# Kernel tuning notes

Hardware: AMD Instinct MI355X
Metric: run time of the kernel (lower is better)

Reference implementation:

```python
import jax, jax.numpy as jnp
import numpy as np

G = 128   # long_term_attn_g
H = 8     # num_attn_heads


def setup_inputs() -> dict:
    key = jax.random.key(0)
    ks = jax.random.split(key, 8)
    b, d, t, dk = 8, 1024, 8192, 512  # dk = model_dim // 2
    return {
        "qk": jax.random.normal(ks[0], (b, d, t), jnp.float32),
        "masks": jnp.ones((b, 1, t), jnp.float32),
        "wq": jax.random.normal(ks[1], (dk, d), jnp.float32) * 0.02,
        "bq": jnp.zeros((dk,), jnp.float32),
        "wk": jax.random.normal(ks[2], (dk, d), jnp.float32) * 0.02,
        "bk": jnp.zeros((dk,), jnp.float32),
        "wv": jax.random.normal(ks[3], (dk, d), jnp.float32) * 0.02,
        "bv": jnp.zeros((dk,), jnp.float32),
        "wo": jax.random.normal(ks[4], (d, dk), jnp.float32) * 0.02,
        "bo": jnp.zeros((d,), jnp.float32),
    }


def _to_patches(x, g):
    # convert_to_patches + rearrange 'b d np p -> (b p) d np'
    b, d, t = x.shape
    pad = (-t) % g
    x = jnp.pad(x, ((0, 0), (0, 0), (0, pad)))
    npat = x.shape[-1] // g
    return x.reshape(b, d, npat, g).transpose(0, 3, 1, 2).reshape(b * g, d, npat)


def reference(qk, masks, wq, bq, wk, bk, wv, bv, wo, bo):
    b, d, t = qk.shape
    xp = _to_patches(qk, G)     # [(b g), d, npat]  -- q, k, v source
    mp = _to_patches(masks, G)  # [(b g), 1, npat]  -- key-side attention mask

    # pointwise Conv1d projections == per-timestep matmuls
    q = jnp.einsum('od,bdt->bot', wq, xp) + bq[:, None]
    k = jnp.einsum('od,bdt->bot', wk, xp) + bk[:, None]
    v = jnp.einsum('od,bdt->bot', wv, xp) + bv[:, None]

    dk = wq.shape[0]
    dh = dk // H
    bg, _, npat = q.shape
    qh = q.reshape(bg, H, dh, npat)
    kh = k.reshape(bg, H, dh, npat)
    vh = v.reshape(bg, H, dh, npat)

    scores = jnp.einsum('bhdi,bhdj->bhij', qh, kh) / jnp.sqrt(jnp.float32(dh))
    scores = jnp.where(mp[:, :, None, :] > 0, scores, jnp.float32(-1e9))
    attn = jax.nn.softmax(scores, axis=-1)
    out = jnp.einsum('bhij,bhdj->bhdi', attn, vh).reshape(bg, dk, npat)

    # out_proj = GELU -> Conv1d(dk -> model_dim, k=1)
    out = jax.nn.gelu(out, approximate=False)
    out = jnp.einsum('od,bdt->bot', wo, out) + bo[:, None]

    # undo reshape: '(b g) d np -> b d (np g)', trim padding
    out = out.reshape(b, G, d, npat).transpose(0, 2, 3, 1).reshape(b, d, npat * G)[:, :, :t]
    return out * masks
```

## Files before the change

kernel.cpp:

```cpp
#include <hip/hip_runtime.h>
#include <hip/hip_bf16.h>
#include <cmath>

typedef __attribute__((ext_vector_type(4))) float f32x4;
typedef __attribute__((ext_vector_type(8))) short s16x8;

typedef __attribute__((address_space(1))) const void glb_void_t;
typedef __attribute__((address_space(3))) void lds_void_t;

#define MFMA(a, b, c) __builtin_amdgcn_mfma_f32_16x16x32_bf16(a, b, c, 0, 0, 0)
#define GLOAD_LDS(g, l) __builtin_amdgcn_global_load_lds((glb_void_t*)(g), (lds_void_t*)(l), 16, 0, 0)

__device__ __forceinline__ unsigned short bf(float x) {
  union { float f; unsigned u; } c; c.f = x;
  unsigned r = (c.u + 0x7fffu + ((c.u >> 16) & 1u)) >> 16;
  return (unsigned short)r;
}

__global__ void k_prep(const float* __restrict__ wq, const float* __restrict__ wk,
                       const float* __restrict__ wv, const float* __restrict__ bq,
                       const float* __restrict__ bk, const float* __restrict__ bv,
                       const float* __restrict__ wo,
                       __hip_bfloat16* __restrict__ wqkv, __hip_bfloat16* __restrict__ wob,
                       float* __restrict__ bqkv) {
  const int NW = 1536 * 1024, NO = 1024 * 512;
  for (int i = blockIdx.x * blockDim.x + threadIdx.x; i < NW + NO + 1536;
       i += gridDim.x * blockDim.x) {
    if (i < NW) {
      int r = i >> 10;
      float v = (r < 512) ? wq[i] : ((r < 1024) ? wk[i - 512 * 1024] : wv[i - 1024 * 1024]);
      ((unsigned short*)wqkv)[i] = bf(v);
    } else if (i < NW + NO) {
      int j = i - NW;
      ((unsigned short*)wob)[j] = bf(wo[j]);
    } else {
      int j = i - NW - NO;
      bqkv[j] = (j < 512) ? bq[j] : ((j < 1024) ? bk[j - 512] : bv[j - 1024]);
    }
  }
}

__global__ __launch_bounds__(256) void k_transpose(const float* __restrict__ qk,
                                                   __hip_bfloat16* __restrict__ qkT) {
  __shared__ float tile[64][65];
  const int b = blockIdx.z, t0 = blockIdx.x * 64, d0 = blockIdx.y * 64;
  const int tid = threadIdx.x;
  const int tq = tid & 15, dr = tid >> 4;
  const float* src = qk + ((size_t)b * 1024 + d0) * 8192 + t0;
#pragma unroll
  for (int i = 0; i < 4; i++) {
    int d = dr + i * 16;
    float4 v = *(const float4*)(src + (size_t)d * 8192 + tq * 4);
    tile[d][tq * 4 + 0] = v.x; tile[d][tq * 4 + 1] = v.y;
    tile[d][tq * 4 + 2] = v.z; tile[d][tq * 4 + 3] = v.w;
  }
  __syncthreads();
  const int d4 = (tid & 15) * 4, tr = tid >> 4;
  unsigned short* dst = (unsigned short*)qkT + ((size_t)b * 8192 + t0) * 1024 + d0;
#pragma unroll
  for (int i = 0; i < 4; i++) {
    int t = tr + i * 16;
    ushort4 o4;
    o4.x = bf(tile[d4 + 0][t]); o4.y = bf(tile[d4 + 1][t]);
    o4.z = bf(tile[d4 + 2][t]); o4.w = bf(tile[d4 + 3][t]);
    *(ushort4*)(dst + (size_t)t * 1024 + d4) = o4;
  }
}

__device__ __forceinline__ void stage_half(char* lds_base, const char* gbase,
                                           int ktile, int w, int l) {
#pragma unroll
  for (int r = 0; r < 2; ++r) {
    int row = r * 64 + w * 8 + (l >> 3);
    int cb = ((l & 7) * 16) ^ ((row & 7) << 4);
    GLOAD_LDS(gbase + (size_t)row * 2048 + (size_t)ktile * 128 + cb,
              lds_base + (r * 64 + w * 8) * 128);
  }
}

__global__ __launch_bounds__(512, 2) void k_qkv(const __hip_bfloat16* __restrict__ qkT,
                                                const __hip_bfloat16* __restrict__ wqkv,
                                                const float* __restrict__ bqkv,
                                                __hip_bfloat16* __restrict__ qkv) {
  __shared__ char smem[131072];
  const int NT = 16;
  const int b = blockIdx.z, t0 = blockIdx.x * 256, o0 = blockIdx.y * 256;
  const int tid = threadIdx.x, l = tid & 63, w = tid >> 6;
  const int c = l & 15, g = l >> 4;
  const int wm = w >> 2, wn = w & 3;
  const int cbase = (g * 16) ^ ((c & 7) << 4);
  const int brow = (wn & 1) * 64;

  const char* qpanel = (const char*)qkT + ((size_t)b * 8192 + t0) * 2048;
  const char* wpanel = (const char*)wqkv + (size_t)o0 * 2048;

#define STAGE_B2(tt) { stage_half(smem + 65536 + ((tt)&1) * 32768, wpanel, (tt), w, l); \
                       stage_half(smem + 65536 + ((tt)&1) * 32768 + 16384, wpanel + 262144, (tt), w, l); }
#define STAGE_A2(tt) { stage_half(smem + ((tt)&1) * 32768, qpanel, (tt), w, l); \
                       stage_half(smem + ((tt)&1) * 32768 + 16384, qpanel + 262144, (tt), w, l); }

  f32x4 acc[8][4];
#pragma unroll
  for (int i = 0; i < 8; i++)
#pragma unroll
    for (int j = 0; j < 4; j++) acc[i][j] = (f32x4){0.f, 0.f, 0.f, 0.f};

  STAGE_B2(0); STAGE_A2(0); STAGE_B2(1); STAGE_A2(1);
  asm volatile("s_waitcnt vmcnt(8)" ::: "memory");
  __builtin_amdgcn_s_barrier();
  __builtin_amdgcn_sched_barrier(0);

  s16x8 avLo[4][2], avHi[4][2], bvLo[2][2], bvHi[2][2];
  {
    const char* Ah = smem + wm * 16384;
    const char* Bh = smem + 65536 + (wn >> 1) * 16384;
#pragma unroll
    for (int mi = 0; mi < 4; ++mi)
#pragma unroll
      for (int kk = 0; kk < 2; ++kk)
        avLo[mi][kk] = *(const s16x8*)(Ah + (mi * 16 + c) * 128 + (cbase ^ (kk << 6)));
#pragma unroll
    for (int ni = 0; ni < 2; ++ni)
#pragma unroll
      for (int kk = 0; kk < 2; ++kk)
        bvLo[ni][kk] = *(const s16x8*)(Bh + (brow + ni * 16 + c) * 128 + (cbase ^ (kk << 6)));
  }

#pragma unroll 2
  for (int t = 0; t < NT; ++t) {
    const int buf = t & 1;
    const char* Ah = smem + buf * 32768 + wm * 16384;
    const char* Bh = smem + 65536 + buf * 32768 + (wn >> 1) * 16384;
    const char* Ah2 = smem + (buf ^ 1) * 32768 + wm * 16384;
    const char* Bh2 = smem + 65536 + (buf ^ 1) * 32768 + (wn >> 1) * 16384;

#pragma unroll
    for (int ni = 0; ni < 2; ++ni)
#pragma unroll
      for (int kk = 0; kk < 2; ++kk)
        bvHi[ni][kk] = *(const s16x8*)(Bh + (brow + (2 + ni) * 16 + c) * 128 + (cbase ^ (kk << 6)));
#pragma unroll
    for (int mi = 0; mi < 2; ++mi)
#pragma unroll
      for (int kk = 0; kk < 2; ++kk)
        avHi[mi][kk] = *(const s16x8*)(Ah + (64 + mi * 16 + c) * 128 + (cbase ^ (kk << 6)));
    __builtin_amdgcn_s_barrier();
    asm volatile("s_waitcnt lgkmcnt(8)" ::: "memory");
    __builtin_amdgcn_sched_barrier(0);
    __builtin_amdgcn_s_setprio(1);
#pragma unroll
    for (int mi = 0; mi < 4; ++mi)
#pragma unroll
      for (int ni = 0; ni < 2; ++ni)
#pragma unroll
        for (int kk = 0; kk < 2; ++kk)
          acc[mi][ni] = MFMA(avLo[mi][kk], bvLo[ni][kk], acc[mi][ni]);
    __builtin_amdgcn_s_setprio(0);
    __builtin_amdgcn_s_barrier();

#pragma unroll
    for (int mi = 2; mi < 4; ++mi)
#pragma unroll
      for (int kk = 0; kk < 2; ++kk)
        avHi[mi][kk] = *(const s16x8*)(Ah + (64 + mi * 16 + c) * 128 + (cbase ^ (kk << 6)));
    __builtin_amdgcn_s_barrier();
    asm volatile("s_waitcnt lgkmcnt(8)" ::: "memory");
    __builtin_amdgcn_sched_barrier(0);
    __builtin_amdgcn_s_setprio(1);
#pragma unroll
    for (int mi = 0; mi < 4; ++mi)
#pragma unroll
      for (int ni = 0; ni < 2; ++ni)
#pragma unroll
        for (int kk = 0; kk < 2; ++kk)
          acc[mi][ni + 2] = MFMA(avLo[mi][kk], bvHi[ni][kk], acc[mi][ni + 2]);
    __builtin_amdgcn_s_setprio(0);
    __builtin_amdgcn_s_barrier();

    if (t + 2 < NT) STAGE_B2(t + 2);
    __builtin_amdgcn_s_barrier();
    asm volatile("s_waitcnt lgkmcnt(0)" ::: "memory");
    __builtin_amdgcn_sched_barrier(0);
    __builtin_amdgcn_s_setprio(1);
#pragma unroll
    for (int mi = 0; mi < 4; ++mi)
#pragma unroll
      for (int ni = 0; ni < 2; ++ni)
#pragma unroll
        for (int kk = 0; kk < 2; ++kk)
          acc[mi + 4][ni] = MFMA(avHi[mi][kk], bvLo[ni][kk], acc[mi + 4][ni]);
    __builtin_amdgcn_s_setprio(0);
    __builtin_amdgcn_s_barrier();

    if (t + 2 < NT) STAGE_A2(t + 2);
    if (t + 2 < NT) {
      asm volatile("s_waitcnt vmcnt(8)" ::: "memory");
    } else {
      asm volatile("s_waitcnt vmcnt(0)" ::: "memory");
    }
    __builtin_amdgcn_s_barrier();
    __builtin_amdgcn_sched_barrier(0);
    if (t + 1 < NT) {
#pragma unroll
      for (int mi = 0; mi < 4; ++mi)
#pragma unroll
        for (int kk = 0; kk < 2; ++kk)
          avLo[mi][kk] = *(const s16x8*)(Ah2 + (mi * 16 + c) * 128 + (cbase ^ (kk << 6)));
#pragma unroll
      for (int ni = 0; ni < 2; ++ni)
#pragma unroll
        for (int kk = 0; kk < 2; ++kk)
          bvLo[ni][kk] = *(const s16x8*)(Bh2 + (brow + ni * 16 + c) * 128 + (cbase ^ (kk << 6)));
    }
    __builtin_amdgcn_s_setprio(1);
#pragma unroll
    for (int mi = 0; mi < 4; ++mi)
#pragma unroll
      for (int ni = 0; ni < 2; ++ni)
#pragma unroll
        for (int kk = 0; kk < 2; ++kk)
          acc[mi + 4][ni + 2] = MFMA(avHi[mi][kk], bvHi[ni][kk], acc[mi + 4][ni + 2]);
    __builtin_amdgcn_s_setprio(0);
    __builtin_amdgcn_s_barrier();
  }
#undef STAGE_A2
#undef STAGE_B2

  unsigned short* outb = (unsigned short*)qkv + ((size_t)b * 8192 + t0) * 1536 + o0;
  float bias[4];
#pragma unroll
  for (int ni = 0; ni < 4; ni++) bias[ni] = bqkv[o0 + wn * 64 + ni * 16 + c];
#pragma unroll
  for (int mi = 0; mi < 8; mi++)
#pragma unroll
    for (int r = 0; r < 4; r++) {
      int t = wm * 128 + mi * 16 + g * 4 + r;
#pragma unroll
      for (int ni = 0; ni < 4; ni++) {
        int o = wn * 64 + ni * 16 + c;
        outb[(size_t)t * 1536 + o] = bf(acc[mi][ni][r] + bias[ni]);
      }
    }
}

__global__ __launch_bounds__(64) void k_attn(const __hip_bfloat16* __restrict__ qkv,
                                             const float* __restrict__ masks,
                                             __hip_bfloat16* __restrict__ a_out) {
  const int l = threadIdx.x, c = l & 15, g = l >> 4;
  const int h = blockIdx.x & 7, bg = blockIdx.x >> 3;
  const int gg = bg & 127, b = bg >> 7;
  const size_t rowstep = (size_t)128 * 1536;
  const __hip_bfloat16* base = qkv + ((size_t)b * 8192 + gg) * 1536 + h * 64;
  const __hip_bfloat16* Qb = base;
  const __hip_bfloat16* Kb = base + 512;
  const __hip_bfloat16* Vb = base + 1024;

  s16x8 kf[4][2], qf[4][2];
#pragma unroll
  for (int f = 0; f < 4; f++)
#pragma unroll
    for (int kk = 0; kk < 2; kk++) {
      size_t roff = (size_t)(f * 16 + c) * rowstep + kk * 32 + g * 8;
      kf[f][kk] = *(const s16x8*)(Kb + roff);
      qf[f][kk] = *(const s16x8*)(Qb + roff);
    }
  f32x4 st[4][4];
#pragma unroll
  for (int i = 0; i < 4; i++)
#pragma unroll
    for (int j = 0; j < 4; j++) st[i][j] = (f32x4){0.f, 0.f, 0.f, 0.f};
#pragma unroll
  for (int mj = 0; mj < 4; mj++)
#pragma unroll
    for (int ni = 0; ni < 4; ni++)
#pragma unroll
      for (int kk = 0; kk < 2; kk++)
        st[mj][ni] = MFMA(kf[mj][kk], qf[ni][kk], st[mj][ni]);

  float mk[4][4];
#pragma unroll
  for (int mj = 0; mj < 4; mj++)
#pragma unroll
    for (int r = 0; r < 4; r++)
      mk[mj][r] = masks[(size_t)b * 8192 + (size_t)(mj * 16 + g * 4 + r) * 128 + gg];

  float inv[4];
#pragma unroll
  for (int ni = 0; ni < 4; ni++) {
    float m = -1e30f;
#pragma unroll
    for (int mj = 0; mj < 4; mj++)
#pragma unroll
      for (int r = 0; r < 4; r++) {
        float s = st[mj][ni][r] * 0.125f;
        s = (mk[mj][r] > 0.f) ? s : -1e9f;
        st[mj][ni][r] = s;
        m = fmaxf(m, s);
      }
    m = fmaxf(m, __shfl_xor(m, 16));
    m = fmaxf(m, __shfl_xor(m, 32));
    float sm = 0.f;
#pragma unroll
    for (int mj = 0; mj < 4; mj++)
#pragma unroll
      for (int r = 0; r < 4; r++) {
        float p = expf(st[mj][ni][r] - m);
        st[mj][ni][r] = p;
        sm += p;
      }
    sm += __shfl_xor(sm, 16);
    sm += __shfl_xor(sm, 32);
    inv[ni] = 1.f / sm;
  }
#pragma unroll
  for (int mj = 0; mj < 4; mj++)
#pragma unroll
    for (int ni = 0; ni < 4; ni++)
#pragma unroll
      for (int r = 0; r < 4; r++) st[mj][ni][r] *= inv[ni];

  unsigned qd[4][4][2];
#pragma unroll
  for (int ni = 0; ni < 4; ni++)
#pragma unroll
    for (int mj = 0; mj < 4; mj++)
#pragma unroll
      for (int wv = 0; wv < 2; wv++)
        qd[ni][mj][wv] = (unsigned)bf(st[mj][ni][2 * wv]) |
                         ((unsigned)bf(st[mj][ni][2 * wv + 1]) << 16);

  f32x4 oacc[4][4];
#pragma unroll
  for (int i = 0; i < 4; i++)
#pragma unroll
    for (int j = 0; j < 4; j++) oacc[i][j] = (f32x4){0.f, 0.f, 0.f, 0.f};

  const int srcA = c + 32 * (g & 1);
  const int srcB = srcA + 16;
  const bool hi = (g >= 2);
#pragma unroll
  for (int kk = 0; kk < 2; kk++) {
    s16x8 af[4];
#pragma unroll
    for (int ni = 0; ni < 4; ni++) {
      unsigned a0 = __shfl(qd[ni][2 * kk][0], srcA);
      unsigned b0 = __shfl(qd[ni][2 * kk + 1][0], srcA);
      unsigned a1 = __shfl(qd[ni][2 * kk][1], srcA);
      unsigned b1 = __shfl(qd[ni][2 * kk + 1][1], srcA);
      unsigned a2 = __shfl(qd[ni][2 * kk][0], srcB);
      unsigned b2 = __shfl(qd[ni][2 * kk + 1][0], srcB);
      unsigned a3 = __shfl(qd[ni][2 * kk][1], srcB);
      unsigned b3 = __shfl(qd[ni][2 * kk + 1][1], srcB);
      union { unsigned u[4]; s16x8 v; } uu;
      uu.u[0] = hi ? b0 : a0;
      uu.u[1] = hi ? b1 : a1;
      uu.u[2] = hi ? b2 : a2;
      uu.u[3] = hi ? b3 : a3;
      af[ni] = uu.v;
    }
    s16x8 bvv[4];
#pragma unroll
    for (int fd = 0; fd < 4; fd++) {
      s16x8 t;
#pragma unroll
      for (int e = 0; e < 8; e++)
        t[e] = *(const short*)(Vb + (size_t)(kk * 32 + g * 8 + e) * rowstep + fd * 16 + c);
      bvv[fd] = t;
    }
#pragma unroll
    for (int fi = 0; fi < 4; fi++)
#pragma unroll
      for (int fd = 0; fd < 4; fd++)
        oacc[fi][fd] = MFMA(af[fi], bvv[fd], oacc[fi][fd]);
  }

  unsigned short* ob = (unsigned short*)a_out + ((size_t)b * 8192 + gg) * 512 + h * 64;
#pragma unroll
  for (int fi = 0; fi < 4; fi++)
#pragma unroll
    for (int fd = 0; fd < 4; fd++)
#pragma unroll
      for (int r = 0; r < 4; r++) {
        float x = oacc[fi][fd][r];
        float ge = 0.5f * x * (1.f + erff(x * 0.70710678118f));
        int i = fi * 16 + g * 4 + r;
        ob[(size_t)i * (128 * 512) + fd * 16 + c] = bf(ge);
      }
}

__global__ __launch_bounds__(512) void k_out(const __hip_bfloat16* __restrict__ wob,
                                             const __hip_bfloat16* __restrict__ a,
                                             const float* __restrict__ bo,
                                             const float* __restrict__ masks,
                                             float* __restrict__ y) {
  __shared__ char smem[256 * 128 + 128 * 128];
  char* As = smem;
  char* Bs = smem + 32768;
  const int b = blockIdx.z, t0 = blockIdx.x * 128, o0 = blockIdx.y * 256;
  const int tid = threadIdx.x, l = tid & 63, w = tid >> 6;
  const int c = l & 15, g = l >> 4;
  const int wm = w >> 1, wn = w & 1;
  const int lrow = l >> 3, lcol = (l & 7) * 16;

  f32x4 acc[4][4];
#pragma unroll
  for (int i = 0; i < 4; i++)
#pragma unroll
    for (int j = 0; j < 4; j++) acc[i][j] = (f32x4){0.f, 0.f, 0.f, 0.f};

  const char* wbase = (const char*)(wob + (size_t)o0 * 512);
  const char* abase = (const char*)(a + ((size_t)b * 8192 + t0) * 512);

  for (int ks = 0; ks < 8; ks++) {
    __syncthreads();
#pragma unroll
    for (int ii = 0; ii < 4; ii++) {
      int row = w * 32 + ii * 8 + lrow;
      int cb = lcol ^ ((row & 7) << 4);
      const char* gp = wbase + (size_t)row * 1024 + ks * 128 + cb;
      GLOAD_LDS(gp, As + (w * 32 + ii * 8) * 128);
    }
#pragma unroll
    for (int ii = 0; ii < 2; ii++) {
      int row = w * 16 + ii * 8 + lrow;
      int cb = lcol ^ ((row & 7) << 4);
      const char* gp = abase + (size_t)row * 1024 + ks * 128 + cb;
      GLOAD_LDS(gp, Bs + (w * 16 + ii * 8) * 128);
    }
    __syncthreads();
#pragma unroll
    for (int kk = 0; kk < 2; kk++) {
      s16x8 av[4], bv[4];
#pragma unroll
      for (int mi = 0; mi < 4; mi++) {
        int row = wm * 64 + mi * 16 + c;
        int cb = (kk * 64 + g * 16) ^ ((row & 7) << 4);
        av[mi] = *(const s16x8*)(As + row * 128 + cb);
      }
#pragma unroll
      for (int ni = 0; ni < 4; ni++) {
        int row = wn * 64 + ni * 16 + c;
        int cb = (kk * 64 + g * 16) ^ ((row & 7) << 4);
        bv[ni] = *(const s16x8*)(Bs + row * 128 + cb);
      }
#pragma unroll
      for (int mi = 0; mi < 4; mi++)
#pragma unroll
        for (int ni = 0; ni < 4; ni++)
          acc[mi][ni] = MFMA(av[mi], bv[ni], acc[mi][ni]);
    }
  }
  int tcol[4];
  float mk[4];
#pragma unroll
  for (int ni = 0; ni < 4; ni++) {
    tcol[ni] = t0 + wn * 64 + ni * 16 + c;
    mk[ni] = masks[(size_t)b * 8192 + tcol[ni]];
  }
#pragma unroll
  for (int mi = 0; mi < 4; mi++)
#pragma unroll
    for (int r = 0; r < 4; r++) {
      int od = o0 + wm * 64 + mi * 16 + g * 4 + r;
      float bias = bo[od];
      float* yrow = y + ((size_t)b * 1024 + od) * 8192;
#pragma unroll
      for (int ni = 0; ni < 4; ni++)
        yrow[tcol[ni]] = (acc[mi][ni][r] + bias) * mk[ni];
    }
}

extern "C" void kernel_launch(void* const* d_in, const int* in_sizes, int n_in,
                              void* d_out, int out_size, void* d_ws, size_t ws_size,
                              hipStream_t stream) {
  const float* qk = (const float*)d_in[0];
  const float* masks = (const float*)d_in[1];
  const float* wq = (const float*)d_in[2];
  const float* bq = (const float*)d_in[3];
  const float* wk = (const float*)d_in[4];
  const float* bk = (const float*)d_in[5];
  const float* wv = (const float*)d_in[6];
  const float* bv = (const float*)d_in[7];
  const float* wo = (const float*)d_in[8];
  const float* bo = (const float*)d_in[9];

  char* ws = (char*)d_ws;
  __hip_bfloat16* qkT = (__hip_bfloat16*)ws;
  __hip_bfloat16* a = (__hip_bfloat16*)ws;
  __hip_bfloat16* wqkv = (__hip_bfloat16*)(ws + 134217728);
  __hip_bfloat16* wob = (__hip_bfloat16*)(ws + 134217728 + 3145728);
  float* bqkv = (float*)(ws + 134217728 + 3145728 + 1048576);

  __hip_bfloat16* qkv = (__hip_bfloat16*)d_out;
  float* y = (float*)d_out;

  k_prep<<<dim3(512), dim3(256), 0, stream>>>(wq, wk, wv, bq, bk, bv, wo, wqkv, wob, bqkv);
  k_transpose<<<dim3(128, 16, 8), dim3(256), 0, stream>>>(qk, qkT);
  k_qkv<<<dim3(32, 6, 8), dim3(512), 0, stream>>>(qkT, wqkv, bqkv, qkv);
  k_attn<<<dim3(8192), dim3(64), 0, stream>>>(qkv, masks, a);
  k_out<<<dim3(64, 4, 8), dim3(512), 0, stream>>>(wob, a, bo, masks, y);
}
```

Before: 471.8 us.

## Load QKV weight fragments directly from global into registers, halving LDS

The QKV projection GEMM no longer stages the weight (B) tile through LDS. Each wave now reads its B fragments straight from global memory into registers, prefetching one k-tile ahead. Only the activation (A) tile stays double-buffered in LDS, so shared memory drops from 128KB to 64KB and the occupancy hint is removed from launch bounds. The pipeline is restructured with fewer barriers and new vmcnt waits, at the cost of global-load latency on the B operand and redundant B reads across waves sharing columns.

```diff
diff --git a/kernel.cpp b/kernel.cpp
--- a/kernel.cpp
+++ b/kernel.cpp
@@ -78,26 +78,25 @@
   }
 }
 
-__global__ __launch_bounds__(512, 2) void k_qkv(const __hip_bfloat16* __restrict__ qkT,
-                                                const __hip_bfloat16* __restrict__ wqkv,
-                                                const float* __restrict__ bqkv,
-                                                __hip_bfloat16* __restrict__ qkv) {
-  __shared__ char smem[131072];
+__global__ __launch_bounds__(512) void k_qkv(const __hip_bfloat16* __restrict__ qkT,
+                                             const __hip_bfloat16* __restrict__ wqkv,
+                                             const float* __restrict__ bqkv,
+                                             __hip_bfloat16* __restrict__ qkv) {
+  __shared__ char smem[65536];
   const int NT = 16;
   const int b = blockIdx.z, t0 = blockIdx.x * 256, o0 = blockIdx.y * 256;
   const int tid = threadIdx.x, l = tid & 63, w = tid >> 6;
   const int c = l & 15, g = l >> 4;
   const int wm = w >> 2, wn = w & 3;
   const int cbase = (g * 16) ^ ((c & 7) << 4);
-  const int brow = (wn & 1) * 64;
 
   const char* qpanel = (const char*)qkT + ((size_t)b * 8192 + t0) * 2048;
   const char* wpanel = (const char*)wqkv + (size_t)o0 * 2048;
-
-#define STAGE_B2(tt) { stage_half(smem + 65536 + ((tt)&1) * 32768, wpanel, (tt), w, l); \
-                       stage_half(smem + 65536 + ((tt)&1) * 32768 + 16384, wpanel + 262144, (tt), w, l); }
-#define STAGE_A2(tt) { stage_half(smem + ((tt)&1) * 32768, qpanel, (tt), w, l); \
-                       stage_half(smem + ((tt)&1) * 32768 + 16384, qpanel + 262144, (tt), w, l); }
+  const char* brow_base = wpanel + (size_t)(wn * 64 + c) * 2048 + g * 16;
+
+#define STAGE_A(tt) { stage_half(smem + ((tt)&1) * 32768, qpanel, (tt), w, l); \
+                      stage_half(smem + ((tt)&1) * 32768 + 16384, qpanel + 262144, (tt), w, l); }
+#define BFRAG(tt, ni, kk) (*(const s16x8*)(brow_base + (size_t)(ni) * (16 * 2048) + (size_t)(tt) * 128 + (kk) * 64))
 
   f32x4 acc[8][4];
 #pragma unroll
@@ -105,48 +104,36 @@
 #pragma unroll
     for (int j = 0; j < 4; j++) acc[i][j] = (f32x4){0.f, 0.f, 0.f, 0.f};
 
-  STAGE_B2(0); STAGE_A2(0); STAGE_B2(1); STAGE_A2(1);
-  asm volatile("s_waitcnt vmcnt(8)" ::: "memory");
+  s16x8 bvLo[2][2], bvHi[2][2];
+#pragma unroll
+  for (int ni = 0; ni < 2; ++ni)
+#pragma unroll
+    for (int kk = 0; kk < 2; ++kk) {
+      bvLo[ni][kk] = BFRAG(0, ni, kk);
+      bvHi[ni][kk] = BFRAG(0, 2 + ni, kk);
+    }
+  __builtin_amdgcn_sched_barrier(0);
+  STAGE_A(0); STAGE_A(1);
+  asm volatile("s_waitcnt vmcnt(4)" ::: "memory");
   __builtin_amdgcn_s_barrier();
-  __builtin_amdgcn_sched_barrier(0);
-
-  s16x8 avLo[4][2], avHi[4][2], bvLo[2][2], bvHi[2][2];
-  {
-    const char* Ah = smem + wm * 16384;
-    const char* Bh = smem + 65536 + (wn >> 1) * 16384;
+
+#pragma unroll 2
+  for (int t = 0; t < NT; ++t) {
+    const char* Ah = smem + (t & 1) * 32768 + wm * 16384;
+
+    s16x8 avLo[4][2], avHi[4][2];
 #pragma unroll
     for (int mi = 0; mi < 4; ++mi)
 #pragma unroll
       for (int kk = 0; kk < 2; ++kk)
         avLo[mi][kk] = *(const s16x8*)(Ah + (mi * 16 + c) * 128 + (cbase ^ (kk << 6)));
-#pragma unroll
-    for (int ni = 0; ni < 2; ++ni)
-#pragma unroll
-      for (int kk = 0; kk < 2; ++kk)
-        bvLo[ni][kk] = *(const s16x8*)(Bh + (brow + ni * 16 + c) * 128 + (cbase ^ (kk << 6)));
-  }
-
-#pragma unroll 2
-  for (int t = 0; t < NT; ++t) {
-    const int buf = t & 1;
-    const char* Ah = smem + buf * 32768 + wm * 16384;
-    const char* Bh = smem + 65536 + buf * 32768 + (wn >> 1) * 16384;
-    const char* Ah2 = smem + (buf ^ 1) * 32768 + wm * 16384;
-    const char* Bh2 = smem + 65536 + (buf ^ 1) * 32768 + (wn >> 1) * 16384;
-
-#pragma unroll
-    for (int ni = 0; ni < 2; ++ni)
-#pragma unroll
-      for (int kk = 0; kk < 2; ++kk)
-        bvHi[ni][kk] = *(const s16x8*)(Bh + (brow + (2 + ni) * 16 + c) * 128 + (cbase ^ (kk << 6)));
-#pragma unroll
-    for (int mi = 0; mi < 2; ++mi)
+    __builtin_amdgcn_sched_barrier(0);
+#pragma unroll
+    for (int mi = 0; mi < 4; ++mi)
 #pragma unroll
       for (int kk = 0; kk < 2; ++kk)
         avHi[mi][kk] = *(const s16x8*)(Ah + (64 + mi * 16 + c) * 128 + (cbase ^ (kk << 6)));
-    __builtin_amdgcn_s_barrier();
-    asm volatile("s_waitcnt lgkmcnt(8)" ::: "memory");
-    __builtin_amdgcn_sched_barrier(0);
+
     __builtin_amdgcn_s_setprio(1);
 #pragma unroll
     for (int mi = 0; mi < 4; ++mi)
@@ -155,18 +142,6 @@
 #pragma unroll
         for (int kk = 0; kk < 2; ++kk)
           acc[mi][ni] = MFMA(avLo[mi][kk], bvLo[ni][kk], acc[mi][ni]);
-    __builtin_amdgcn_s_setprio(0);
-    __builtin_amdgcn_s_barrier();
-
-#pragma unroll
-    for (int mi = 2; mi < 4; ++mi)
-#pragma unroll
-      for (int kk = 0; kk < 2; ++kk)
-        avHi[mi][kk] = *(const s16x8*)(Ah + (64 + mi * 16 + c) * 128 + (cbase ^ (kk << 6)));
-    __builtin_amdgcn_s_barrier();
-    asm volatile("s_waitcnt lgkmcnt(8)" ::: "memory");
-    __builtin_amdgcn_sched_barrier(0);
-    __builtin_amdgcn_s_setprio(1);
 #pragma unroll
     for (int mi = 0; mi < 4; ++mi)
 #pragma unroll
@@ -174,14 +149,6 @@
 #pragma unroll
         for (int kk = 0; kk < 2; ++kk)
           acc[mi][ni + 2] = MFMA(avLo[mi][kk], bvHi[ni][kk], acc[mi][ni + 2]);
-    __builtin_amdgcn_s_setprio(0);
-    __builtin_amdgcn_s_barrier();
-
-    if (t + 2 < NT) STAGE_B2(t + 2);
-    __builtin_amdgcn_s_barrier();
-    asm volatile("s_waitcnt lgkmcnt(0)" ::: "memory");
-    __builtin_amdgcn_sched_barrier(0);
-    __builtin_amdgcn_s_setprio(1);
 #pragma unroll
     for (int mi = 0; mi < 4; ++mi)
 #pragma unroll
@@ -190,28 +157,18 @@
         for (int kk = 0; kk < 2; ++kk)
           acc[mi + 4][ni] = MFMA(avHi[mi][kk], bvLo[ni][kk], acc[mi + 4][ni]);
     __builtin_amdgcn_s_setprio(0);
+
+    if (t + 1 < NT) {
+#pragma unroll
+      for (int ni = 0; ni < 2; ++ni)
+#pragma unroll
+        for (int kk = 0; kk < 2; ++kk)
+          bvLo[ni][kk] = BFRAG(t + 1, ni, kk);
+    }
+
     __builtin_amdgcn_s_barrier();
-
-    if (t + 2 < NT) STAGE_A2(t + 2);
-    if (t + 2 < NT) {
-      asm volatile("s_waitcnt vmcnt(8)" ::: "memory");
-    } else {
-      asm volatile("s_waitcnt vmcnt(0)" ::: "memory");
-    }
-    __builtin_amdgcn_s_barrier();
-    __builtin_amdgcn_sched_barrier(0);
-    if (t + 1 < NT) {
-#pragma unroll
-      for (int mi = 0; mi < 4; ++mi)
-#pragma unroll
-        for (int kk = 0; kk < 2; ++kk)
-          avLo[mi][kk] = *(const s16x8*)(Ah2 + (mi * 16 + c) * 128 + (cbase ^ (kk << 6)));
-#pragma unroll
-      for (int ni = 0; ni < 2; ++ni)
-#pragma unroll
-        for (int kk = 0; kk < 2; ++kk)
-          bvLo[ni][kk] = *(const s16x8*)(Bh2 + (brow + ni * 16 + c) * 128 + (cbase ^ (kk << 6)));
-    }
+    if (t + 2 < NT) STAGE_A(t + 2);
+
     __builtin_amdgcn_s_setprio(1);
 #pragma unroll
     for (int mi = 0; mi < 4; ++mi)
@@ -221,10 +178,26 @@
         for (int kk = 0; kk < 2; ++kk)
           acc[mi + 4][ni + 2] = MFMA(avHi[mi][kk], bvHi[ni][kk], acc[mi + 4][ni + 2]);
     __builtin_amdgcn_s_setprio(0);
-    __builtin_amdgcn_s_barrier();
-  }
-#undef STAGE_A2
-#undef STAGE_B2
+
+    if (t + 1 < NT) {
+#pragma unroll
+      for (int ni = 0; ni < 2; ++ni)
+#pragma unroll
+        for (int kk = 0; kk < 2; ++kk)
+          bvHi[ni][kk] = BFRAG(t + 1, 2 + ni, kk);
+    }
+
+    if (t < NT - 1) {
+      if (t == 0 || t + 2 >= NT) {
+        asm volatile("s_waitcnt vmcnt(12)" ::: "memory");
+      } else {
+        asm volatile("s_waitcnt vmcnt(16)" ::: "memory");
+      }
+      __builtin_amdgcn_s_barrier();
+    }
+  }
+#undef STAGE_A
+#undef BFRAG
 
   unsigned short* outb = (unsigned short*)qkv + ((size_t)b * 8192 + t0) * 1536 + o0;
   float bias[4];
```

After: 560.4 us. +18.8%, slower.
